# Kernel tuning notes

Measured on AMD Instinct MI355X. Metric: run time of the kernel, lower is better.

## Reference

```python
import jax, jax.numpy as jnp
import numpy as np

B, D, H, W = 1, 4, 48, 48
C, NH = 256, 8
HD = C // NH
KD, KH, KW = 3, 5, 5
KVOL = KD * KH * KW
SCALE = HD ** -0.5


def _nbhd(L, k):
    """Neighborhood start indices (clamped to stay in-bounds, natten semantics)
    and relative-position-bias indices for one axis."""
    i = jnp.arange(L)
    start = jnp.clip(i - k // 2, 0, L - k)            # [L]
    idx = start[:, None] + jnp.arange(k)[None, :]     # [L,k] absolute neighbor index
    rel = idx - i[:, None] + (k - 1)                  # [L,k] rpb index in [0, 2k-2]
    return idx, rel


def setup_inputs() -> dict:
    key = jax.random.key(0)
    ks = jax.random.split(key, 5)
    s = 0.02
    return {
        "x": jax.random.normal(ks[0], (B, D, H, W, C), jnp.float32),
        "w_qkv": jax.random.normal(ks[1], (C, 3 * C), jnp.float32) * s,
        "b_qkv": jnp.zeros((3 * C,), jnp.float32),
        "rpb": jax.random.normal(ks[2], (NH, 2 * KD - 1, 2 * KH - 1, 2 * KW - 1), jnp.float32) * s,
        "w_proj": jax.random.normal(ks[3], (C, C), jnp.float32) * s,
        "b_proj": jnp.zeros((C,), jnp.float32),
    }


def _nat3d(q, k, v, rpb):
    # q,k,v: [B,NH,D,H,W,HD]; q already scaled
    idxD, relD = _nbhd(D, KD)
    idxH, relH = _nbhd(H, KH)
    idxW, relW = _nbhd(W, KW)
    iD = idxD[:, None, None, :, None, None]
    iH = idxH[None, :, None, None, :, None]
    iW = idxW[None, None, :, None, None, :]
    gk = k[:, :, iD, iH, iW]   # [B,NH,D,H,W,KD,KH,KW,HD]
    gv = v[:, :, iD, iH, iW]
    bias = rpb[:, relD[:, None, None, :, None, None],
                  relH[None, :, None, None, :, None],
                  relW[None, None, :, None, None, :]]  # [NH,D,H,W,KD,KH,KW]
    scores = jnp.einsum("bndyxc,bndyxtuvc->bndyxtuv", q, gk) + bias[None]
    flat = scores.reshape(*scores.shape[:5], KVOL)
    attn = jax.nn.softmax(flat, axis=-1).reshape(scores.shape)
    return jnp.einsum("bndyxtuv,bndyxtuvc->bndyxc", attn, gv)


def reference(x, w_qkv, b_qkv, rpb, w_proj, b_proj):
    qkv = (x @ w_qkv + b_qkv).reshape(B, D, H, W, 3, NH, HD)
    qkv = jnp.transpose(qkv, (4, 0, 5, 1, 2, 3, 6))  # [3,B,NH,D,H,W,HD]
    q, k, v = qkv[0] * SCALE, qkv[1], qkv[2]
    out = _nat3d(q, k, v, rpb)                       # [B,NH,D,H,W,HD]
    out = jnp.transpose(out, (0, 2, 3, 4, 1, 5)).reshape(B, D, H, W, C)
    return out @ w_proj + b_proj
```

## Files before the change

### kernel.cpp

```cpp
#include <hip/hip_runtime.h>

#define QK_SCALE 0.17677669529663687f
#define TOKENS 9216

typedef __attribute__((ext_vector_type(8))) __bf16 bf16x8;
typedef __attribute__((ext_vector_type(8))) unsigned short us8;
typedef __attribute__((ext_vector_type(4))) float f32x4;

static __device__ __forceinline__ unsigned short f2bf(float x) {
    unsigned int u = __float_as_uint(x);
    return (unsigned short)((u + 0x7FFFu + ((u >> 16) & 1u)) >> 16);
}
static __device__ __forceinline__ bf16x8 ld_bf8(const unsigned short* p) {
    us8 u = *reinterpret_cast<const us8*>(p);
    return __builtin_bit_cast(bf16x8, u);
}

__global__ __launch_bounds__(256) void conv_prep(
    const float* __restrict__ x, const float* __restrict__ wqkv, const float* __restrict__ wproj,
    unsigned short* __restrict__ xb, unsigned short* __restrict__ wqT, unsigned short* __restrict__ wpT)
{
    int b = blockIdx.x, t = threadIdx.x;
    if (b < 2304) {
        int idx = (b * 256 + t) * 4;
        float4 v = *reinterpret_cast<const float4*>(x + idx);
        ushort4 o;
        o.x = f2bf(v.x); o.y = f2bf(v.y); o.z = f2bf(v.z); o.w = f2bf(v.w);
        *reinterpret_cast<ushort4*>(xb + idx) = o;
    } else if (b < 3072) {
        int e = (b - 2304) * 256 + t;
        int n = e >> 8, k = e & 255;
        wqT[n * 256 + k] = f2bf(wqkv[k * 768 + n]);
    } else {
        int e = (b - 3072) * 256 + t;
        int n = e >> 8, k = e & 255;
        wpT[n * 256 + k] = f2bf(wproj[k * 256 + n]);
    }
}

template<int MF, int NF, int MODE>
__global__ __launch_bounds__(256) void gemm_mfma(
    const unsigned short* __restrict__ A, const unsigned short* __restrict__ BT,
    const float* __restrict__ bias,
    unsigned short* __restrict__ oq, unsigned short* __restrict__ ok,
    unsigned short* __restrict__ ov, float* __restrict__ of)
{
    const int tid = threadIdx.x;
    const int wid = tid >> 6, lane = tid & 63;
    const int wm = wid >> 1, wn = wid & 1;
    const int n15 = lane & 15, g = lane >> 4;
    const int m0 = blockIdx.y * (MF * 32) + wm * (MF * 16);
    const int n0 = blockIdx.x * (NF * 32) + wn * (NF * 16);

    f32x4 acc[MF][NF];
    #pragma unroll
    for (int i = 0; i < MF; i++)
        #pragma unroll
        for (int j = 0; j < NF; j++)
            acc[i][j] = f32x4{0.f, 0.f, 0.f, 0.f};

    #pragma unroll
    for (int ks = 0; ks < 8; ++ks) {
        bf16x8 a[MF], b[NF];
        #pragma unroll
        for (int mt = 0; mt < MF; ++mt)
            a[mt] = ld_bf8(A + (size_t)(m0 + mt * 16 + n15) * 256 + ks * 32 + g * 8);
        #pragma unroll
        for (int nt = 0; nt < NF; ++nt)
            b[nt] = ld_bf8(BT + (size_t)(n0 + nt * 16 + n15) * 256 + ks * 32 + g * 8);
        #pragma unroll
        for (int mt = 0; mt < MF; ++mt)
            #pragma unroll
            for (int nt = 0; nt < NF; ++nt)
                acc[mt][nt] = __builtin_amdgcn_mfma_f32_16x16x32_bf16(a[mt], b[nt], acc[mt][nt], 0, 0, 0);
    }

    #pragma unroll
    for (int mt = 0; mt < MF; ++mt) {
        #pragma unroll
        for (int nt = 0; nt < NF; ++nt) {
            int col = n0 + nt * 16 + n15;
            float bv = bias[col];
            #pragma unroll
            for (int rg = 0; rg < 4; ++rg) {
                int row = m0 + mt * 16 + g * 4 + rg;
                float val = acc[mt][nt][rg] + bv;
                if (MODE == 0) {
                    int part = col >> 8, c = col & 255, hh = c >> 5, ch = c & 31;
                    unsigned short* dst = (part == 0) ? oq : ((part == 1) ? ok : ov);
                    if (part == 0) val *= QK_SCALE;
                    dst[((size_t)hh * TOKENS + row) * 32 + ch] = f2bf(val);
                } else {
                    of[(size_t)row * 256 + col] = val;
                }
            }
        }
    }
}

__global__ __launch_bounds__(128) void nat_attn_mfma(
    const unsigned short* __restrict__ qws, const unsigned short* __restrict__ kws,
    const unsigned short* __restrict__ vws, const float* __restrict__ rpb,
    unsigned short* __restrict__ aout)
{
    __shared__ unsigned short VT[32 * 200];
    __shared__ unsigned short Pl[16 * 200];
    __shared__ float biasL[405];
    __shared__ float red[2][16][2];

    const int tid = threadIdx.x;
    const int w = tid >> 6, lane = tid & 63;
    const int n15 = lane & 15, g = lane >> 4;

    int b = blockIdx.x;
    const int h = b & 7; b >>= 3;
    const int bx = b % 12; b /= 12;
    const int by = b % 12;
    const int d  = b / 12;
    const int y0 = by * 4, x0 = bx * 4;
    const int base_d = min(max(d - 1, 0), 1);
    const int base_h = min(max(y0 - 2, 0), 40);
    const int base_w = min(max(x0 - 2, 0), 40);
    const int relD = base_d - d + 2;

    const size_t hoff = (size_t)h * TOKENS * 32;
    const unsigned short* kb = kws + hoff;
    const unsigned short* vb = vws + hoff;
    const unsigned short* qb = qws + hoff;

    for (int i = tid; i < 405; i += 128) biasL[i] = rpb[h * 405 + i];

    for (int id = tid; id < 768; id += 128) {
        int cand = id % 192, chg = id / 192;
        int ld = cand >> 6, lh = (cand >> 3) & 7, lw = cand & 7;
        int gt = (base_d + ld) * 2304 + (base_h + lh) * 48 + (base_w + lw);
        us8 u = *reinterpret_cast<const us8*>(vb + (size_t)gt * 32 + chg * 8);
        #pragma unroll
        for (int e = 0; e < 8; e++) VT[(chg * 8 + e) * 200 + cand] = u[e];
    }
    __syncthreads();

    const int gtq = d * 2304 + (y0 + (n15 >> 2)) * 48 + (x0 + (n15 & 3));
    bf16x8 qf = ld_bf8(qb + (size_t)gtq * 32 + g * 8);

    f32x4 sf[6];
    #pragma unroll
    for (int i = 0; i < 6; ++i) {
        int cand = (w * 6 + i) * 16 + n15;
        int ld = cand >> 6, lh = (cand >> 3) & 7, lw = cand & 7;
        int gtc = (base_d + ld) * 2304 + (base_h + lh) * 48 + (base_w + lw);
        bf16x8 kf = ld_bf8(kb + (size_t)gtc * 32 + g * 8);
        sf[i] = __builtin_amdgcn_mfma_f32_16x16x32_bf16(qf, kf, f32x4{0.f, 0.f, 0.f, 0.f}, 0, 0, 0);
    }

    int shl[4], swl[4], oy[4], ox[4], gtr[4];
    #pragma unroll
    for (int rg = 0; rg < 4; ++rg) {
        int tok = g * 4 + rg;
        int y = y0 + (tok >> 2), x = x0 + (tok & 3);
        int sh = min(max(y - 2, 0), 43), sw = min(max(x - 2, 0), 43);
        shl[rg] = sh - base_h; swl[rg] = sw - base_w;
        oy[rg] = y - base_h;   ox[rg] = x - base_w;
        gtr[rg] = d * 2304 + y * 48 + x;
    }

    float ev[6][4], mw[4], sm[4];
    #pragma unroll
    for (int rg = 0; rg < 4; ++rg) {
        float mx = -1e30f;
        #pragma unroll
        for (int i = 0; i < 6; ++i) {
            int cand = (w * 6 + i) * 16 + n15;
            int ld = cand >> 6, lh = (cand >> 3) & 7, lw = cand & 7;
            int t0 = lh - shl[rg], t1 = lw - swl[rg];
            bool valid = ((unsigned)t0 < 5u) && ((unsigned)t1 < 5u);
            int bi = (relD + ld) * 81 + (lh - oy[rg] + 4) * 9 + (lw - ox[rg] + 4);
            float bvv = biasL[valid ? bi : 0];
            float sc = valid ? (sf[i][rg] + bvv) : -1e30f;
            ev[i][rg] = sc;
            mx = fmaxf(mx, sc);
        }
        #pragma unroll
        for (int msk = 1; msk < 16; msk <<= 1) mx = fmaxf(mx, __shfl_xor(mx, msk));
        float ssum = 0.f;
        #pragma unroll
        for (int i = 0; i < 6; ++i) {
            float ee = __expf(ev[i][rg] - mx);
            ev[i][rg] = ee;
            ssum += ee;
        }
        #pragma unroll
        for (int msk = 1; msk < 16; msk <<= 1) ssum += __shfl_xor(ssum, msk);
        mw[rg] = mx; sm[rg] = ssum;
    }
    if (n15 == 0) {
        #pragma unroll
        for (int rg = 0; rg < 4; ++rg) {
            red[w][g * 4 + rg][0] = mw[rg];
            red[w][g * 4 + rg][1] = sm[rg];
        }
    }
    __syncthreads();

    float fac[4];
    #pragma unroll
    for (int rg = 0; rg < 4; ++rg) {
        int tk = g * 4 + rg;
        float m0_ = red[0][tk][0], s0_ = red[0][tk][1];
        float m1_ = red[1][tk][0], s1_ = red[1][tk][1];
        float m = fmaxf(m0_, m1_);
        float tot = s0_ * __expf(m0_ - m) + s1_ * __expf(m1_ - m);
        fac[rg] = __expf(mw[rg] - m) / tot;
    }
    #pragma unroll
    for (int rg = 0; rg < 4; ++rg)
        #pragma unroll
        for (int i = 0; i < 6; ++i)
            Pl[(g * 4 + rg) * 200 + (w * 6 + i) * 16 + n15] = f2bf(ev[i][rg] * fac[rg]);
    __syncthreads();

    f32x4 oacc = f32x4{0.f, 0.f, 0.f, 0.f};
    #pragma unroll
    for (int ks = 0; ks < 6; ++ks) {
        bf16x8 pa = ld_bf8(&Pl[n15 * 200 + ks * 32 + g * 8]);
        bf16x8 vf = ld_bf8(&VT[(w * 16 + n15) * 200 + ks * 32 + g * 8]);
        oacc = __builtin_amdgcn_mfma_f32_16x16x32_bf16(pa, vf, oacc, 0, 0, 0);
    }
    #pragma unroll
    for (int rg = 0; rg < 4; ++rg)
        aout[(size_t)gtr[rg] * 256 + h * 32 + w * 16 + n15] = f2bf(oacc[rg]);
}

extern "C" void kernel_launch(void* const* d_in, const int* in_sizes, int n_in,
                              void* d_out, int out_size, void* d_ws, size_t ws_size,
                              hipStream_t stream) {
    const float* x      = (const float*)d_in[0];
    const float* w_qkv  = (const float*)d_in[1];
    const float* b_qkv  = (const float*)d_in[2];
    const float* rpb    = (const float*)d_in[3];
    const float* w_proj = (const float*)d_in[4];
    const float* b_proj = (const float*)d_in[5];
    float* out = (float*)d_out;

    unsigned short* ws = (unsigned short*)d_ws;
    unsigned short* xb    = ws;
    unsigned short* wqT   = ws + (size_t)2359296;
    unsigned short* wpT   = ws + (size_t)2555904;
    unsigned short* qws   = ws + (size_t)2621440;
    unsigned short* kws   = ws + (size_t)4980736;
    unsigned short* vws   = ws + (size_t)7340032;
    unsigned short* aws   = ws + (size_t)9699328;

    conv_prep<<<dim3(3328), 256, 0, stream>>>(x, w_qkv, w_proj, xb, wqT, wpT);

    gemm_mfma<4, 4, 0><<<dim3(6, 72), 256, 0, stream>>>(xb, wqT, b_qkv, qws, kws, vws, nullptr);

    nat_attn_mfma<<<dim3(4608), 128, 0, stream>>>(qws, kws, vws, rpb, aws);

    gemm_mfma<2, 2, 1><<<dim3(4, 144), 256, 0, stream>>>(aws, wpT, b_proj, nullptr, nullptr, nullptr, out);
}
```

Measured before the change: 70.28 us.

## Precompute masked per-class bias tables and shrink QKV GEMM tile

Adds a prep kernel that builds bf16 bias tables for each boundary class, depth and head, with -inf already written for invalid neighbors. The attention kernel then loads per-lane bias straight from global memory instead of staging rpb in shared memory and doing index and validity arithmetic per score. The __syncthreads is moved after the QK MFMAs to overlap them with the V transpose. The QKV GEMM tile is also narrowed to NF=2, doubling the grid. This trades an extra small kernel launch and more global bias reads for less ALU work, and rounds the bias to bf16, which slightly changes precision.

```diff
diff --git a/kernel.cpp b/kernel.cpp
--- a/kernel.cpp
+++ b/kernel.cpp
@@ -10,6 +10,9 @@
 static __device__ __forceinline__ unsigned short f2bf(float x) {
     unsigned int u = __float_as_uint(x);
     return (unsigned short)((u + 0x7FFFu + ((u >> 16) & 1u)) >> 16);
+}
+static __device__ __forceinline__ float bf2f(unsigned short u) {
+    return __uint_as_float(((unsigned int)u) << 16);
 }
 static __device__ __forceinline__ bf16x8 ld_bf8(const unsigned short* p) {
     us8 u = *reinterpret_cast<const us8*>(p);
@@ -35,6 +38,39 @@
         int e = (b - 3072) * 256 + t;
         int n = e >> 8, k = e & 255;
         wpT[n * 256 + k] = f2bf(wproj[k * 256 + n]);
+    }
+}
+
+__global__ __launch_bounds__(256) void prep_bias(
+    const float* __restrict__ rpb, unsigned short* __restrict__ biasT)
+{
+    const int bid = blockIdx.x;
+    const int cls = bid >> 3, h = bid & 7;
+    const int d  = cls / 9;
+    const int r  = cls % 9;
+    const int yc = r / 3, xc = r % 3;
+    const int by = (yc == 0) ? 0 : ((yc == 1) ? 5 : 11);
+    const int bx = (xc == 0) ? 0 : ((xc == 1) ? 5 : 11);
+    const int y0 = by * 4, x0 = bx * 4;
+    const int base_d = min(max(d - 1, 0), 1);
+    const int base_h = min(max(y0 - 2, 0), 40);
+    const int base_w = min(max(x0 - 2, 0), 40);
+    const int relD = base_d - d + 2;
+    unsigned short* dst = biasT + (size_t)bid * 3072;
+
+    for (int idx = threadIdx.x; idx < 3072; idx += 256) {
+        int tok = idx / 192, cand = idx % 192;
+        int y = y0 + (tok >> 2), x = x0 + (tok & 3);
+        int sh = min(max(y - 2, 0), 43), sw = min(max(x - 2, 0), 43);
+        int ld = cand >> 6, lh = (cand >> 3) & 7, lw = cand & 7;
+        int t0 = lh - (sh - base_h), t1 = lw - (sw - base_w);
+        bool valid = ((unsigned)t0 < 5u) && ((unsigned)t1 < 5u);
+        unsigned short v = 0xFF80;
+        if (valid) {
+            int bi = (relD + ld) * 81 + (lh - (y - base_h) + 4) * 9 + (lw - (x - base_w) + 4);
+            v = f2bf(rpb[h * 405 + bi]);
+        }
+        dst[idx] = v;
     }
 }
 
@@ -100,12 +136,11 @@
 
 __global__ __launch_bounds__(128) void nat_attn_mfma(
     const unsigned short* __restrict__ qws, const unsigned short* __restrict__ kws,
-    const unsigned short* __restrict__ vws, const float* __restrict__ rpb,
+    const unsigned short* __restrict__ vws, const unsigned short* __restrict__ biasT,
     unsigned short* __restrict__ aout)
 {
     __shared__ unsigned short VT[32 * 200];
     __shared__ unsigned short Pl[16 * 200];
-    __shared__ float biasL[405];
     __shared__ float red[2][16][2];
 
     const int tid = threadIdx.x;
@@ -121,14 +156,15 @@
     const int base_d = min(max(d - 1, 0), 1);
     const int base_h = min(max(y0 - 2, 0), 40);
     const int base_w = min(max(x0 - 2, 0), 40);
-    const int relD = base_d - d + 2;
+
+    const int yc = (by == 0) ? 0 : ((by == 11) ? 2 : 1);
+    const int xc = (bx == 0) ? 0 : ((bx == 11) ? 2 : 1);
+    const unsigned short* bT = biasT + (size_t)(((d * 9 + yc * 3 + xc) * 8 + h)) * 3072;
 
     const size_t hoff = (size_t)h * TOKENS * 32;
     const unsigned short* kb = kws + hoff;
     const unsigned short* vb = vws + hoff;
     const unsigned short* qb = qws + hoff;
-
-    for (int i = tid; i < 405; i += 128) biasL[i] = rpb[h * 405 + i];
 
     for (int id = tid; id < 768; id += 128) {
         int cand = id % 192, chg = id / 192;
@@ -138,7 +174,13 @@
         #pragma unroll
         for (int e = 0; e < 8; e++) VT[(chg * 8 + e) * 200 + cand] = u[e];
     }
-    __syncthreads();
+
+    float bvv[6][4];
+    #pragma unroll
+    for (int i = 0; i < 6; ++i)
+        #pragma unroll
+        for (int rg = 0; rg < 4; ++rg)
+            bvv[i][rg] = bf2f(bT[(g * 4 + rg) * 192 + w * 96 + i * 16 + n15]);
 
     const int gtq = d * 2304 + (y0 + (n15 >> 2)) * 48 + (x0 + (n15 & 3));
     bf16x8 qf = ld_bf8(qb + (size_t)gtq * 32 + g * 8);
@@ -152,16 +194,13 @@
         bf16x8 kf = ld_bf8(kb + (size_t)gtc * 32 + g * 8);
         sf[i] = __builtin_amdgcn_mfma_f32_16x16x32_bf16(qf, kf, f32x4{0.f, 0.f, 0.f, 0.f}, 0, 0, 0);
     }
-
-    int shl[4], swl[4], oy[4], ox[4], gtr[4];
+    __syncthreads();
+
+    int gtr[4];
     #pragma unroll
     for (int rg = 0; rg < 4; ++rg) {
         int tok = g * 4 + rg;
-        int y = y0 + (tok >> 2), x = x0 + (tok & 3);
-        int sh = min(max(y - 2, 0), 43), sw = min(max(x - 2, 0), 43);
-        shl[rg] = sh - base_h; swl[rg] = sw - base_w;
-        oy[rg] = y - base_h;   ox[rg] = x - base_w;
-        gtr[rg] = d * 2304 + y * 48 + x;
+        gtr[rg] = d * 2304 + (y0 + (tok >> 2)) * 48 + (x0 + (tok & 3));
     }
 
     float ev[6][4], mw[4], sm[4];
@@ -170,13 +209,7 @@
         float mx = -1e30f;
         #pragma unroll
         for (int i = 0; i < 6; ++i) {
-            int cand = (w * 6 + i) * 16 + n15;
-            int ld = cand >> 6, lh = (cand >> 3) & 7, lw = cand & 7;
-            int t0 = lh - shl[rg], t1 = lw - swl[rg];
-            bool valid = ((unsigned)t0 < 5u) && ((unsigned)t1 < 5u);
-            int bi = (relD + ld) * 81 + (lh - oy[rg] + 4) * 9 + (lw - ox[rg] + 4);
-            float bvv = biasL[valid ? bi : 0];
-            float sc = valid ? (sf[i][rg] + bvv) : -1e30f;
+            float sc = sf[i][rg] + bvv[i][rg];
             ev[i][rg] = sc;
             mx = fmaxf(mx, sc);
         }
@@ -250,12 +283,14 @@
     unsigned short* kws   = ws + (size_t)4980736;
     unsigned short* vws   = ws + (size_t)7340032;
     unsigned short* aws   = ws + (size_t)9699328;
+    unsigned short* biasT = ws + (size_t)12058624;
 
     conv_prep<<<dim3(3328), 256, 0, stream>>>(x, w_qkv, w_proj, xb, wqT, wpT);
-
-    gemm_mfma<4, 4, 0><<<dim3(6, 72), 256, 0, stream>>>(xb, wqT, b_qkv, qws, kws, vws, nullptr);
-
-    nat_attn_mfma<<<dim3(4608), 128, 0, stream>>>(qws, kws, vws, rpb, aws);
+    prep_bias<<<dim3(288), 256, 0, stream>>>(rpb, biasT);
+
+    gemm_mfma<4, 2, 0><<<dim3(12, 72), 256, 0, stream>>>(xb, wqT, b_qkv, qws, kws, vws, nullptr);
+
+    nat_attn_mfma<<<dim3(4608), 128, 0, stream>>>(qws, kws, vws, biasT, aws);
 
     gemm_mfma<2, 2, 1><<<dim3(4, 144), 256, 0, stream>>>(aws, wpT, b_proj, nullptr, nullptr, nullptr, out);
 }
```

After: 74.82 us. 6.5% more time.
